# Performance work log

Hardware: AMD Instinct MI355X
Metric: run time of the kernel (lower is better)

## Reference

```python
import jax, jax.numpy as jnp
import numpy as np

NUM_CLASS = 4
K = 512
TEMP = 0.1
NEG_BIG = -1e9


def setup_inputs() -> dict:
    key = jax.random.key(0)
    ks = jax.random.split(key, 7)
    B, D, H, W = 8, 128, 128, 128
    return {
        "feat_x": jax.random.normal(ks[0], (B, D, H, W), jnp.float32),
        "pred_gt": jax.random.randint(ks[1], (B, H, W), 0, NUM_CLASS),
        "gt": jax.random.randint(ks[2], (B, H, W), 0, NUM_CLASS),
        "feat_u_s": jax.random.normal(ks[3], (B, D, H, W), jnp.float32),
        "feat_u_fp": jax.random.normal(ks[4], (B, D, H, W), jnp.float32),
        "logits_u": jax.random.uniform(ks[5], (B, H, W), jnp.float32),
        "label_u": jax.random.randint(ks[6], (B, H, W), 0, NUM_CLASS),
    }


def _rank_of_valid(mask, key):
    # Per-position rank under a random permutation; valid pixels get ranks [0, nv).
    r = jax.random.uniform(key, mask.shape)
    keys = jnp.where(mask, r, 2.0)  # invalid pixels sort last
    order = jnp.argsort(keys)
    return jnp.zeros_like(order).at[order].set(jnp.arange(order.shape[0]))


def _sample_feats(f_flat, mask, n, key):
    # f_flat: [N, D], mask: [N] bool -> feats [n+1, D] (n samples + class mean), valid [n+1]
    nv = mask.sum()
    order = jnp.argsort(jnp.where(mask, 0, 1))  # stable: valid pixel positions first
    u = jax.random.uniform(key, (n,))
    rand_idx = jnp.floor(u * nv).astype(jnp.int32)            # sample w/ replacement
    rep_idx = (jnp.arange(n) % jnp.maximum(nv, 1)).astype(jnp.int32)  # cyclic repeat
    idx = jnp.where(nv >= n, rand_idx, rep_idx)
    sampled = f_flat[order[idx]]                              # [n, D]
    mean = (f_flat * mask[:, None]).sum(0) / jnp.maximum(nv, 1)
    feats = jnp.concatenate([sampled, mean[None]], axis=0)
    valid = jnp.full((n + 1,), True) & (nv > 0)
    return feats, valid


def reference(feat_x, pred_gt, gt, feat_u_s, feat_u_fp, logits_u, label_u):
    # Label maps already at feature resolution -> nearest/bilinear resizes are identity.
    B, D, H, W = feat_x.shape
    N = B * H * W
    key = jax.random.key(42)
    base, rem = K // NUM_CLASS, K % NUM_CLASS

    f_l = feat_x.transpose(0, 2, 3, 1).reshape(N, D)
    f_s = feat_u_s.transpose(0, 2, 3, 1).reshape(N, D)
    f_fp = feat_u_fp.transpose(0, 2, 3, 1).reshape(N, D)
    pred_flat = pred_gt.reshape(N)
    lab_u_flat = label_u.reshape(N)
    log_u_flat = logits_u.reshape(N)
    thr = log_u_flat.mean()  # use_threshold=False -> dynamic mean threshold

    feats_l, valid_l, labels_l = [], [], []
    feats_u, valid_u, labels_u = [], [], []
    for cls in range(NUM_CLASS):
        n = base + (rem if cls == NUM_CLASS - 1 else 0)
        key, k1, k2, k3, k4 = jax.random.split(key, 5)
        # labeled: mask = pred == cls (use_TP=False)
        ml = pred_flat == cls
        fl, vl = _sample_feats(f_l, ml, n, k1)
        feats_l.append(fl); valid_l.append(vl)
        labels_l.append(jnp.full((n + 1,), cls, jnp.int32))
        # unlabeled: confident pixels of this class, randomly split into s / fp halves
        mu = (lab_u_flat == cls) & (log_u_flat >= thr)
        ranks = _rank_of_valid(mu, k2)
        half = mu.sum() // 2
        ms = mu & (ranks < half)
        mfp = mu & (ranks >= half)
        fs, vs = _sample_feats(f_s, ms, n, k3)
        ffp, vfp = _sample_feats(f_fp, mfp, n, k4)
        feats_u += [fs, ffp]; valid_u += [vs, vfp]
        labels_u.append(jnp.full((2 * (n + 1),), cls, jnp.int32))

    feat_l = jnp.concatenate(feats_l); val_l = jnp.concatenate(valid_l)
    lab_l = jnp.concatenate(labels_l)
    feat_u = jnp.concatenate(feats_u); val_u = jnp.concatenate(valid_u)
    labs_u = jnp.concatenate(labels_u)

    # InfoNCE over valid anchors/contrasts (validity mask replaces torch's NaN-row filtering)
    logits = feat_l @ feat_u.T / TEMP                      # [Kl, Ku]
    logits = jnp.where(val_u[None, :], logits, NEG_BIG)
    logits = logits - jax.lax.stop_gradient(logits.max(axis=1, keepdims=True))
    log_denom = jnp.log(jnp.exp(logits).sum(axis=1, keepdims=True))
    log_prob = jnp.where(val_u[None, :], logits - log_denom, 0.0)
    pos = ((lab_l[:, None] == labs_u[None, :]) & val_u[None, :]).astype(feat_l.dtype)
    mean_lpp = (pos * log_prob).sum(axis=1) / (pos.sum(axis=1) + 1e-12)
    loss = -(mean_lpp * val_l).sum() / jnp.maximum(val_l.sum(), 1)
    return jnp.where(val_l.any() & val_u.any(), loss, 0.0)
```

## Files before the change

### kernel.cpp

```cpp
#include <hip/hip_runtime.h>
#include <stdint.h>

#define N_PIX 131072
#define HW 16384
#define NSAMP 128
#define GSZ 129
#define ROWS_L 516
#define COLS_U 1032
#define INVALID_M 0xFFFFFFFFu

__host__ __device__ inline void tf2x32(uint32_t k0, uint32_t k1,
                                       uint32_t x0, uint32_t x1,
                                       uint32_t& o0, uint32_t& o1) {
  uint32_t ks2 = k0 ^ k1 ^ 0x1BD11BDAu;
  x0 += k0; x1 += k1;
#define TFR(r) { x0 += x1; x1 = (x1 << (r)) | (x1 >> (32 - (r))); x1 ^= x0; }
  TFR(13) TFR(15) TFR(26) TFR(6)   x0 += k1;  x1 += ks2 + 1u;
  TFR(17) TFR(29) TFR(16) TFR(24)  x0 += ks2; x1 += k0 + 2u;
  TFR(13) TFR(15) TFR(26) TFR(6)   x0 += k0;  x1 += k1 + 3u;
  TFR(17) TFR(29) TFR(16) TFR(24)  x0 += k1;  x1 += ks2 + 4u;
  TFR(13) TFR(15) TFR(26) TFR(6)   x0 += ks2; x1 += k0 + 5u;
#undef TFR
  o0 = x0; o1 = x1;
}

struct Keys4  { uint32_t a[4];  uint32_t b[4];  };
struct Keys12 { uint32_t a[12]; uint32_t b[12]; };

__global__ void k_sum(const float* __restrict__ x, double* out) {
  __shared__ double sm[256];
  int t = threadIdx.x;
  int base = blockIdx.x * 1024;
  double v = (double)x[base + t] + (double)x[base + 256 + t]
           + (double)x[base + 512 + t] + (double)x[base + 768 + t];
  sm[t] = v; __syncthreads();
  for (int o = 128; o > 0; o >>= 1) { if (t < o) sm[t] += sm[t + o]; __syncthreads(); }
  if (t == 0) atomicAdd(out, sm[0]);
}

__global__ void k_rankbits(const int* __restrict__ lab, const float* __restrict__ logu,
                           const double* __restrict__ sum, unsigned* __restrict__ m,
                           unsigned* __restrict__ cntu, Keys4 k2) {
  __shared__ unsigned cnt[4];
  int t = threadIdx.x;
  if (t < 4) cnt[t] = 0u;
  __syncthreads();
  int j = blockIdx.x * blockDim.x + t;
  double thr = (*sum) / 131072.0;
  int i0 = j, i1 = j + 65536;
  unsigned m0 = INVALID_M, m1 = INVALID_M;
  uint32_t o0, o1;
  if ((double)logu[i0] >= thr) {
    int c = lab[i0];
    tf2x32(k2.a[c], k2.b[c], (uint32_t)j, (uint32_t)(j + 65536), o0, o1);
    m0 = o0 >> 9; atomicAdd(&cnt[c], 1u);
  }
  if ((double)logu[i1] >= thr) {
    int c = lab[i1];
    tf2x32(k2.a[c], k2.b[c], (uint32_t)j, (uint32_t)(j + 65536), o0, o1);
    m1 = o1 >> 9; atomicAdd(&cnt[c], 1u);
  }
  m[i0] = m0; m[i1] = m1;
  __syncthreads();
  if (t < 4 && cnt[t] > 0u) atomicAdd(&cntu[t], cnt[t]);
}

__global__ void k_hist1(const int* __restrict__ lab, const unsigned* __restrict__ m,
                        unsigned* __restrict__ hist1) {
  int i = blockIdx.x * 256 + threadIdx.x;
  unsigned mi = m[i];
  if (mi != INVALID_M) atomicAdd(&hist1[lab[i] * 4096 + (mi >> 11)], 1u);
}

__global__ void k_scan1(const unsigned* __restrict__ hist1, const unsigned* __restrict__ cntu,
                        int* __restrict__ half_, int* __restrict__ bin_, int* __restrict__ base_) {
  int c = blockIdx.x, t = threadIdx.x;
  __shared__ unsigned part[256];
  const unsigned* h = hist1 + c * 4096;
  unsigned s = 0;
  for (int k = 0; k < 16; k++) s += h[t * 16 + k];
  part[t] = s; __syncthreads();
  if (t == 0) {
    int half = (int)(cntu[c] / 2u); half_[c] = half;
    if (half <= 0) { bin_[c] = -1; base_[c] = 0; }
    else {
      unsigned target = (unsigned)(half - 1), cum = 0; int pb = 0;
      for (; pb < 256; pb++) { if (cum + part[pb] > target) break; cum += part[pb]; }
      int b = pb * 16;
      for (;; b++) { unsigned hb = h[b]; if (cum + hb > target) break; cum += hb; }
      bin_[c] = b; base_[c] = (int)cum;
    }
  }
}

__global__ void k_hist2(const int* __restrict__ lab, const unsigned* __restrict__ m,
                        const int* __restrict__ bin_, unsigned* __restrict__ hist2) {
  int i = blockIdx.x * 256 + threadIdx.x;
  unsigned mi = m[i];
  if (mi == INVALID_M) return;
  int c = lab[i];
  if ((int)(mi >> 11) == bin_[c]) atomicAdd(&hist2[c * 2048 + (mi & 0x7FFu)], 1u);
}

__global__ void k_scan2(const unsigned* __restrict__ hist2, const int* __restrict__ half_,
                        const int* __restrict__ base_, const int* __restrict__ bin_,
                        unsigned* __restrict__ mstar_, int* __restrict__ t_) {
  int c = blockIdx.x, t = threadIdx.x;
  __shared__ unsigned part[256];
  const unsigned* h = hist2 + c * 2048;
  unsigned s = 0;
  for (int k = 0; k < 8; k++) s += h[t * 8 + k];
  part[t] = s; __syncthreads();
  if (t == 0) {
    int half = half_[c];
    if (half <= 0) { mstar_[c] = 0u; t_[c] = 0; }
    else {
      unsigned target = (unsigned)(half - 1), cum = (unsigned)base_[c]; int pb = 0;
      for (; pb < 256; pb++) { if (cum + part[pb] > target) break; cum += part[pb]; }
      int v = pb * 8;
      for (;; v++) { unsigned hb = h[v]; if (cum + hb > target) break; cum += hb; }
      mstar_[c] = ((unsigned)bin_[c] << 11) | (unsigned)v;
      t_[c] = half - (int)cum;
    }
  }
}

__global__ void k_ties(const int* __restrict__ lab, const unsigned* __restrict__ m,
                       const unsigned* __restrict__ mstar_, int* __restrict__ tiecnt,
                       int* __restrict__ tielist) {
  int i = blockIdx.x * 256 + threadIdx.x;
  unsigned mi = m[i];
  if (mi == INVALID_M) return;
  int c = lab[i];
  if (mi == mstar_[c]) {
    int p = atomicAdd(&tiecnt[c], 1);
    if (p < 128) tielist[c * 128 + p] = i;
  }
}

__global__ void k_tiesort(int* __restrict__ tielist, const int* __restrict__ tiecnt) {
  int c = threadIdx.x; if (c >= 4) return;
  int n = tiecnt[c]; if (n > 128) n = 128;
  int* L = tielist + c * 128;
  for (int a = 1; a < n; a++) {
    int x = L[a]; int b = a - 1;
    while (b >= 0 && L[b] > x) { L[b + 1] = L[b]; b--; }
    L[b + 1] = x;
  }
}

__global__ void k_split(const int* __restrict__ pred, const int* __restrict__ lab,
                        const unsigned* __restrict__ m, const unsigned* __restrict__ mstar_,
                        const int* __restrict__ t_, const int* __restrict__ tielist,
                        const int* __restrict__ tiecnt,
                        uint8_t* __restrict__ lgid, uint8_t* __restrict__ ugid,
                        unsigned* __restrict__ bc) {
  __shared__ unsigned cnt[12];
  int t = threadIdx.x;
  int i = blockIdx.x * 128 + t;
  if (t < 12) cnt[t] = 0u;
  __syncthreads();
  int pc = pred[i];
  lgid[i] = (uint8_t)pc;
  atomicAdd(&cnt[pc], 1u);
  unsigned mi = m[i];
  uint8_t ug = 255;
  if (mi != INVALID_M) {
    int c = lab[i];
    unsigned ms = mstar_[c];
    bool in_s;
    if (mi < ms) in_s = true;
    else if (mi > ms) in_s = false;
    else {
      int tc = tiecnt[c]; if (tc > 128) tc = 128;
      const int* L = tielist + c * 128;
      int rk = 0;
      for (int a = 0; a < tc; a++) if (L[a] < i) rk++;
      in_s = (rk < t_[c]);
    }
    ug = (uint8_t)((c << 1) + (in_s ? 0 : 1));
    atomicAdd(&cnt[4 + ug], 1u);
  }
  ugid[i] = ug;
  __syncthreads();
  if (t < 12) bc[t * 1024 + blockIdx.x] = cnt[t];
}

__global__ void k_scanblocks(const unsigned* __restrict__ bc, unsigned* __restrict__ offs,
                             unsigned* __restrict__ tot) {
  __shared__ unsigned wsum[16];
  int t = threadIdx.x;
  int lane = t & 63, w = t >> 6;
  for (int g = 0; g < 12; g++) {
    unsigned v = bc[g * 1024 + t];
    unsigned x = v;
    for (int o = 1; o < 64; o <<= 1) {
      unsigned y = __shfl_up(x, o, 64);
      if (lane >= o) x += y;
    }
    if (lane == 63) wsum[w] = x;
    __syncthreads();
    if (w == 0 && lane < 16) {
      unsigned s = wsum[lane];
      for (int o = 1; o < 16; o <<= 1) {
        unsigned y = __shfl_up(s, o, 64);
        if (lane >= o) s += y;
      }
      wsum[lane] = s;
    }
    __syncthreads();
    unsigned base = (w > 0) ? wsum[w - 1] : 0u;
    offs[g * 1024 + t] = base + x - v;
    if (t == 1023) tot[g] = base + x;
    __syncthreads();
  }
}

__global__ void k_sample(Keys12 gk, const unsigned* __restrict__ offs,
                         const unsigned* __restrict__ tot,
                         const uint8_t* __restrict__ lgid, const uint8_t* __restrict__ ugid,
                         int* __restrict__ sel) {
  int g = blockIdx.x, s = threadIdx.x;
  int nv = (int)tot[g];
  if (nv <= 0) { sel[g * 128 + s] = 0; return; }
  uint32_t o0, o1; int jj = s & 63;
  tf2x32(gk.a[g], gk.b[g], (uint32_t)jj, (uint32_t)(jj + 64), o0, o1);
  uint32_t bits = (s < 64) ? o0 : o1;
  float u = __uint_as_float((bits >> 9) | 0x3f800000u) - 1.0f;
  int q = (nv >= NSAMP) ? (int)floorf(u * (float)nv) : (s % nv);
  if (q > nv - 1) q = nv - 1;
  const unsigned* of = offs + g * 1024;
  int lo = 0, hi = 1023;
  while (lo < hi) { int mid = (lo + hi + 1) >> 1; if (of[mid] <= (unsigned)q) lo = mid; else hi = mid - 1; }
  int rem = q - (int)of[lo];
  const uint8_t* arr = (g < 4) ? lgid : ugid;
  uint8_t want = (g < 4) ? (uint8_t)g : (uint8_t)(g - 4);
  const unsigned* w32 = (const unsigned*)(arr + lo * 128);
  unsigned buf[32];
#pragma unroll
  for (int k = 0; k < 32; k++) buf[k] = w32[k];
  int found = 0;
  for (int k = 0; k < 128; k++) {
    uint8_t bb = (uint8_t)(buf[k >> 2] >> ((k & 3) * 8));
    if (bb == want) { if (rem == 0) { found = lo * 128 + k; break; } rem--; }
  }
  sel[g * 128 + s] = found;
}

__global__ void k_means(const float* __restrict__ fx, const float* __restrict__ fs,
                        const float* __restrict__ ffp,
                        const uint8_t* __restrict__ lgid, const uint8_t* __restrict__ ugid,
                        float* __restrict__ gsum) {
  int tensor = blockIdx.y;
  const float* f = (tensor == 0) ? fx : ((tensor == 1) ? fs : ffp);
  int b = blockIdx.x >> 7, d = blockIdx.x & 127;
  int t = threadIdx.x;
  int lane = t & 63, w = t >> 6;
  const float4* row4 = (const float4*)(f + ((size_t)(b * 128 + d)) * HW);
  const uchar4* gid4 = (const uchar4*)((tensor == 0 ? lgid : ugid) + (size_t)b * HW);
  int par = tensor - 1;
  float a0 = 0.f, a1 = 0.f, a2 = 0.f, a3 = 0.f;
#pragma unroll
  for (int i = 0; i < 16; i++) {
    int idx = i * 256 + t;
    float4 v = row4[idx];
    uchar4 gg = gid4[idx];
    int s0, s1, s2, s3;
    if (tensor == 0) { s0 = gg.x; s1 = gg.y; s2 = gg.z; s3 = gg.w; }
    else {
      s0 = (gg.x != 255 && (gg.x & 1) == par) ? (gg.x >> 1) : -1;
      s1 = (gg.y != 255 && (gg.y & 1) == par) ? (gg.y >> 1) : -1;
      s2 = (gg.z != 255 && (gg.z & 1) == par) ? (gg.z >> 1) : -1;
      s3 = (gg.w != 255 && (gg.w & 1) == par) ? (gg.w >> 1) : -1;
    }
    a0 += ((s0 == 0) ? v.x : 0.f) + ((s1 == 0) ? v.y : 0.f) + ((s2 == 0) ? v.z : 0.f) + ((s3 == 0) ? v.w : 0.f);
    a1 += ((s0 == 1) ? v.x : 0.f) + ((s1 == 1) ? v.y : 0.f) + ((s2 == 1) ? v.z : 0.f) + ((s3 == 1) ? v.w : 0.f);
    a2 += ((s0 == 2) ? v.x : 0.f) + ((s1 == 2) ? v.y : 0.f) + ((s2 == 2) ? v.z : 0.f) + ((s3 == 2) ? v.w : 0.f);
    a3 += ((s0 == 3) ? v.x : 0.f) + ((s1 == 3) ? v.y : 0.f) + ((s2 == 3) ? v.z : 0.f) + ((s3 == 3) ? v.w : 0.f);
  }
  for (int o = 32; o > 0; o >>= 1) {
    a0 += __shfl_xor(a0, o, 64);
    a1 += __shfl_xor(a1, o, 64);
    a2 += __shfl_xor(a2, o, 64);
    a3 += __shfl_xor(a3, o, 64);
  }
  __shared__ float swsum[4][4];
  if (lane == 0) { swsum[w][0] = a0; swsum[w][1] = a1; swsum[w][2] = a2; swsum[w][3] = a3; }
  __syncthreads();
  if (t < 4) {
    float v = swsum[0][t] + swsum[1][t] + swsum[2][t] + swsum[3][t];
    int g = (tensor == 0) ? t : (4 + (t << 1) + par);
    atomicAdd(&gsum[g * 128 + d], v);
  }
}

__global__ void k_gather(const float* __restrict__ fx, const float* __restrict__ fs,
                         const float* __restrict__ ffp, const int* __restrict__ sel,
                         const float* __restrict__ gsum, const unsigned* __restrict__ tot,
                         float* __restrict__ featl, float* __restrict__ featuT) {
  int r = blockIdx.x, d = threadIdx.x;
  const float* src; int g, s;
  if (r < ROWS_L) { g = r / GSZ; s = r - g * GSZ; src = fx; }
  else {
    int col = r - ROWS_L; int gu = col / GSZ; s = col - gu * GSZ;
    g = 4 + gu; src = (gu & 1) ? ffp : fs;
  }
  float val;
  if (s == NSAMP) {
    int nv = (int)tot[g]; if (nv < 1) nv = 1;
    val = gsum[g * 128 + d] / (float)nv;
  } else {
    int p = sel[g * 128 + s];
    int b = p >> 14, hw = p & 16383;
    val = src[((size_t)(b * 128 + d)) * HW + hw];
  }
  if (r < ROWS_L) featl[r * 128 + d] = val;
  else featuT[d * COLS_U + (r - ROWS_L)] = val;
}

__global__ void k_loss(const float* __restrict__ featl, const float* __restrict__ featuT,
                       const unsigned* __restrict__ tot, float* __restrict__ rowv) {
  int r = blockIdx.x, t = threadIdx.x;
  __shared__ float srow[128];
  __shared__ float slog[COLS_U];
  __shared__ float red[256];
  __shared__ float sbc[2];
  if (t < 128) srow[t] = featl[r * 128 + t];
  __syncthreads();
  for (int j = t; j < COLS_U; j += 256) {
    int gu = j / GSZ;
    float v;
    if (tot[4 + gu] > 0u) {
      float acc = 0.f;
      for (int d = 0; d < 128; d++) acc += srow[d] * featuT[d * COLS_U + j];
      v = acc / 0.1f;
    } else v = -1e9f;
    slog[j] = v;
  }
  __syncthreads();
  float mx = -3.4e38f;
  for (int j = t; j < COLS_U; j += 256) mx = fmaxf(mx, slog[j]);
  red[t] = mx; __syncthreads();
  for (int o = 128; o > 0; o >>= 1) { if (t < o) red[t] = fmaxf(red[t], red[t + o]); __syncthreads(); }
  if (t == 0) sbc[0] = red[0];
  __syncthreads();
  mx = sbc[0];
  float se = 0.f;
  for (int j = t; j < COLS_U; j += 256) se += expf(slog[j] - mx);
  red[t] = se; __syncthreads();
  for (int o = 128; o > 0; o >>= 1) { if (t < o) red[t] += red[t + o]; __syncthreads(); }
  if (t == 0) sbc[1] = logf(red[0]);
  __syncthreads();
  float logden = sbc[1];
  int myc = r / GSZ;
  float ps = 0.f, pl = 0.f;
  for (int j = t; j < COLS_U; j += 256) {
    int gu = j / GSZ;
    if (tot[4 + gu] > 0u && (gu >> 1) == myc) { ps += 1.f; pl += slog[j] - mx - logden; }
  }
  red[t] = ps; __syncthreads();
  for (int o = 128; o > 0; o >>= 1) { if (t < o) red[t] += red[t + o]; __syncthreads(); }
  float pst = red[0]; __syncthreads();
  red[t] = pl; __syncthreads();
  for (int o = 128; o > 0; o >>= 1) { if (t < o) red[t] += red[t + o]; __syncthreads(); }
  if (t == 0) rowv[r] = red[0] / (pst + 1e-12f);
}

__global__ void k_final(const float* __restrict__ rowv, const unsigned* __restrict__ tot,
                        float* __restrict__ out) {
  __shared__ float red[256];
  __shared__ float redc[256];
  int t = threadIdx.x;
  float s = 0.f, cn = 0.f;
  for (int r = t; r < ROWS_L; r += 256) {
    if (tot[r / GSZ] > 0u) { s += rowv[r]; cn += 1.f; }
  }
  red[t] = s; redc[t] = cn; __syncthreads();
  for (int o = 128; o > 0; o >>= 1) {
    if (t < o) { red[t] += red[t + o]; redc[t] += redc[t + o]; }
    __syncthreads();
  }
  if (t == 0) {
    bool anyL = (tot[0] | tot[1] | tot[2] | tot[3]) > 0u;
    bool anyU = false;
    for (int g = 4; g < 12; g++) anyU = anyU || (tot[g] > 0u);
    float loss = -red[0] / fmaxf(redc[0], 1.f);
    out[0] = (anyL && anyU) ? loss : 0.f;
  }
}

extern "C" void kernel_launch(void* const* d_in, const int* in_sizes, int n_in,
                              void* d_out, int out_size, void* d_ws, size_t ws_size,
                              hipStream_t stream) {
  const float* fx   = (const float*)d_in[0];
  const int*   pred = (const int*)d_in[1];
  const float* fs   = (const float*)d_in[3];
  const float* ffp  = (const float*)d_in[4];
  const float* logu = (const float*)d_in[5];
  const int*   lab  = (const int*)d_in[6];
  float* out = (float*)d_out;
  char* w = (char*)d_ws;

  uint32_t ka = 0u, kb = 42u;
  Keys4 K2; Keys12 GK;
  for (int c = 0; c < 4; c++) {
    uint32_t X0[5], X1[5];
    for (int j = 0; j < 5; j++) tf2x32(ka, kb, (uint32_t)j, (uint32_t)(j + 5), X0[j], X1[j]);
    uint32_t fl[10] = {X0[0],X0[1],X0[2],X0[3],X0[4],X1[0],X1[1],X1[2],X1[3],X1[4]};
    ka = fl[0]; kb = fl[1];
    GK.a[c] = fl[2];        GK.b[c] = fl[3];
    K2.a[c] = fl[4];        K2.b[c] = fl[5];
    GK.a[4 + 2*c] = fl[6];  GK.b[4 + 2*c] = fl[7];
    GK.a[5 + 2*c] = fl[8];  GK.b[5 + 2*c] = fl[9];
  }

  double*   d_sum    = (double*)(w + 0);
  unsigned* d_cntu   = (unsigned*)(w + 64);
  int*      d_half   = (int*)(w + 128);
  int*      d_bin    = (int*)(w + 192);
  int*      d_base   = (int*)(w + 256);
  unsigned* d_mstar  = (unsigned*)(w + 320);
  int*      d_tt     = (int*)(w + 384);
  int*      d_tiecnt = (int*)(w + 448);
  int*      d_tielist= (int*)(w + 512);
  unsigned* d_hist1  = (unsigned*)(w + 4096);
  unsigned* d_hist2  = (unsigned*)(w + 69632);
  unsigned* d_tot    = (unsigned*)(w + 102400);
  unsigned* d_bc     = (unsigned*)(w + 102656);
  unsigned* d_offs   = (unsigned*)(w + 151808);
  int*      d_sel    = (int*)(w + 200960);
  float*    d_gsum   = (float*)(w + 207104);
  unsigned* d_m      = (unsigned*)(w + 213248);
  uint8_t*  d_lgid   = (uint8_t*)(w + 737536);
  uint8_t*  d_ugid   = (uint8_t*)(w + 868608);
  float*    d_featl  = (float*)(w + 999680);
  float*    d_featuT = (float*)(w + 1263872);
  float*    d_rowv   = (float*)(w + 1792256);

  hipMemsetAsync(w, 0, 102400, stream);
  hipMemsetAsync(d_gsum, 0, 6144, stream);

  k_sum<<<128, 256, 0, stream>>>(logu, d_sum);
  k_rankbits<<<256, 256, 0, stream>>>(lab, logu, d_sum, d_m, d_cntu, K2);
  k_hist1<<<512, 256, 0, stream>>>(lab, d_m, d_hist1);
  k_scan1<<<4, 256, 0, stream>>>(d_hist1, d_cntu, d_half, d_bin, d_base);
  k_hist2<<<512, 256, 0, stream>>>(lab, d_m, d_bin, d_hist2);
  k_scan2<<<4, 256, 0, stream>>>(d_hist2, d_half, d_base, d_bin, d_mstar, d_tt);
  k_ties<<<512, 256, 0, stream>>>(lab, d_m, d_mstar, d_tiecnt, d_tielist);
  k_tiesort<<<1, 64, 0, stream>>>(d_tielist, d_tiecnt);
  k_split<<<1024, 128, 0, stream>>>(pred, lab, d_m, d_mstar, d_tt, d_tielist, d_tiecnt,
                                    d_lgid, d_ugid, d_bc);
  k_scanblocks<<<1, 1024, 0, stream>>>(d_bc, d_offs, d_tot);
  k_sample<<<12, 128, 0, stream>>>(GK, d_offs, d_tot, d_lgid, d_ugid, d_sel);
  k_means<<<dim3(1024, 3), 256, 0, stream>>>(fx, fs, ffp, d_lgid, d_ugid, d_gsum);
  k_gather<<<ROWS_L + COLS_U, 128, 0, stream>>>(fx, fs, ffp, d_sel, d_gsum, d_tot,
                                                d_featl, d_featuT);
  k_loss<<<ROWS_L, 256, 0, stream>>>(d_featl, d_featuT, d_tot, d_rowv);
  k_final<<<1, 256, 0, stream>>>(d_rowv, d_tot, out);
  (void)in_sizes; (void)n_in; (void)out_size; (void)ws_size;
}
```

Measured before the change: 340.7 us.

## Fuse pipeline stages with last-block-done reductions to cut kernel launches

Merges the histogram, scan, tie handling, block scan and sampling kernels into three kernels, each finishing with a last-block epilogue chosen by an atomic counter. The final loss reduction moves into the loss kernel the same way. The means kernel is split across twice as many blocks for more parallelism. The goal is to remove many small serial kernel launches and dependent round trips. In exchange, the tail work now runs serially in a single block, and the loss reductions switch to double precision.

```diff
diff --git a/kernel.cpp b/kernel.cpp
--- a/kernel.cpp
+++ b/kernel.cpp
@@ -27,6 +27,18 @@
 struct Keys4  { uint32_t a[4];  uint32_t b[4];  };
 struct Keys12 { uint32_t a[12]; uint32_t b[12]; };
 
+__device__ __forceinline__ bool last_block(unsigned* ctr, unsigned nblocks) {
+  __shared__ unsigned rk_;
+  __threadfence();
+  __syncthreads();
+  if (threadIdx.x == 0)
+    rk_ = __hip_atomic_fetch_add(ctr, 1u, __ATOMIC_ACQ_REL, __HIP_MEMORY_SCOPE_AGENT);
+  __syncthreads();
+  if (rk_ != nblocks - 1u) return false;
+  __threadfence();
+  return true;
+}
+
 __global__ void k_sum(const float* __restrict__ x, double* out) {
   __shared__ double sm[256];
   int t = threadIdx.x;
@@ -38,14 +50,16 @@
   if (t == 0) atomicAdd(out, sm[0]);
 }
 
-__global__ void k_rankbits(const int* __restrict__ lab, const float* __restrict__ logu,
-                           const double* __restrict__ sum, unsigned* __restrict__ m,
-                           unsigned* __restrict__ cntu, Keys4 k2) {
+__global__ void k_rank(const int* __restrict__ lab, const float* __restrict__ logu,
+                       const double* __restrict__ sum, unsigned* __restrict__ m,
+                       unsigned* __restrict__ cntu, unsigned* __restrict__ hist1,
+                       int* __restrict__ half_, int* __restrict__ bin_,
+                       int* __restrict__ base_, unsigned* __restrict__ ctr, Keys4 k2) {
   __shared__ unsigned cnt[4];
   int t = threadIdx.x;
   if (t < 4) cnt[t] = 0u;
   __syncthreads();
-  int j = blockIdx.x * blockDim.x + t;
+  int j = blockIdx.x * 256 + t;
   double thr = (*sum) / 131072.0;
   int i0 = j, i1 = j + 65536;
   unsigned m0 = INVALID_M, m1 = INVALID_M;
@@ -54,197 +68,195 @@
     int c = lab[i0];
     tf2x32(k2.a[c], k2.b[c], (uint32_t)j, (uint32_t)(j + 65536), o0, o1);
     m0 = o0 >> 9; atomicAdd(&cnt[c], 1u);
+    atomicAdd(&hist1[c * 4096 + (m0 >> 11)], 1u);
   }
   if ((double)logu[i1] >= thr) {
     int c = lab[i1];
     tf2x32(k2.a[c], k2.b[c], (uint32_t)j, (uint32_t)(j + 65536), o0, o1);
     m1 = o1 >> 9; atomicAdd(&cnt[c], 1u);
+    atomicAdd(&hist1[c * 4096 + (m1 >> 11)], 1u);
   }
   m[i0] = m0; m[i1] = m1;
   __syncthreads();
   if (t < 4 && cnt[t] > 0u) atomicAdd(&cntu[t], cnt[t]);
-}
-
-__global__ void k_hist1(const int* __restrict__ lab, const unsigned* __restrict__ m,
-                        unsigned* __restrict__ hist1) {
-  int i = blockIdx.x * 256 + threadIdx.x;
+
+  if (!last_block(ctr, gridDim.x)) return;
+  __shared__ unsigned part[256];
+  for (int c = 0; c < 4; c++) {
+    const unsigned* h = hist1 + c * 4096;
+    unsigned s = 0;
+    for (int k = 0; k < 16; k++) s += h[t * 16 + k];
+    part[t] = s; __syncthreads();
+    if (t == 0) {
+      int half = (int)(cntu[c] / 2u); half_[c] = half;
+      if (half <= 0) { bin_[c] = -1; base_[c] = 0; }
+      else {
+        unsigned target = (unsigned)(half - 1), cum = 0; int pb = 0;
+        for (; pb < 256; pb++) { if (cum + part[pb] > target) break; cum += part[pb]; }
+        int b = pb * 16;
+        for (;; b++) { unsigned hb = h[b]; if (cum + hb > target) break; cum += hb; }
+        bin_[c] = b; base_[c] = (int)cum;
+      }
+    }
+    __syncthreads();
+  }
+}
+
+__global__ void k_h2s2(const int* __restrict__ lab, const unsigned* __restrict__ m,
+                       const int* __restrict__ bin_, unsigned* __restrict__ hist2,
+                       const int* __restrict__ half_, const int* __restrict__ base_,
+                       unsigned* __restrict__ mstar_, int* __restrict__ t_,
+                       unsigned* __restrict__ ctr) {
+  int t = threadIdx.x;
+  int i = blockIdx.x * 256 + t;
   unsigned mi = m[i];
-  if (mi != INVALID_M) atomicAdd(&hist1[lab[i] * 4096 + (mi >> 11)], 1u);
-}
-
-__global__ void k_scan1(const unsigned* __restrict__ hist1, const unsigned* __restrict__ cntu,
-                        int* __restrict__ half_, int* __restrict__ bin_, int* __restrict__ base_) {
-  int c = blockIdx.x, t = threadIdx.x;
+  if (mi != INVALID_M) {
+    int c = lab[i];
+    if ((int)(mi >> 11) == bin_[c]) atomicAdd(&hist2[c * 2048 + (mi & 0x7FFu)], 1u);
+  }
+  if (!last_block(ctr, gridDim.x)) return;
   __shared__ unsigned part[256];
-  const unsigned* h = hist1 + c * 4096;
-  unsigned s = 0;
-  for (int k = 0; k < 16; k++) s += h[t * 16 + k];
-  part[t] = s; __syncthreads();
-  if (t == 0) {
-    int half = (int)(cntu[c] / 2u); half_[c] = half;
-    if (half <= 0) { bin_[c] = -1; base_[c] = 0; }
-    else {
-      unsigned target = (unsigned)(half - 1), cum = 0; int pb = 0;
-      for (; pb < 256; pb++) { if (cum + part[pb] > target) break; cum += part[pb]; }
-      int b = pb * 16;
-      for (;; b++) { unsigned hb = h[b]; if (cum + hb > target) break; cum += hb; }
-      bin_[c] = b; base_[c] = (int)cum;
-    }
-  }
-}
-
-__global__ void k_hist2(const int* __restrict__ lab, const unsigned* __restrict__ m,
-                        const int* __restrict__ bin_, unsigned* __restrict__ hist2) {
-  int i = blockIdx.x * 256 + threadIdx.x;
-  unsigned mi = m[i];
-  if (mi == INVALID_M) return;
-  int c = lab[i];
-  if ((int)(mi >> 11) == bin_[c]) atomicAdd(&hist2[c * 2048 + (mi & 0x7FFu)], 1u);
-}
-
-__global__ void k_scan2(const unsigned* __restrict__ hist2, const int* __restrict__ half_,
-                        const int* __restrict__ base_, const int* __restrict__ bin_,
-                        unsigned* __restrict__ mstar_, int* __restrict__ t_) {
-  int c = blockIdx.x, t = threadIdx.x;
-  __shared__ unsigned part[256];
-  const unsigned* h = hist2 + c * 2048;
-  unsigned s = 0;
-  for (int k = 0; k < 8; k++) s += h[t * 8 + k];
-  part[t] = s; __syncthreads();
-  if (t == 0) {
-    int half = half_[c];
-    if (half <= 0) { mstar_[c] = 0u; t_[c] = 0; }
-    else {
-      unsigned target = (unsigned)(half - 1), cum = (unsigned)base_[c]; int pb = 0;
-      for (; pb < 256; pb++) { if (cum + part[pb] > target) break; cum += part[pb]; }
-      int v = pb * 8;
-      for (;; v++) { unsigned hb = h[v]; if (cum + hb > target) break; cum += hb; }
-      mstar_[c] = ((unsigned)bin_[c] << 11) | (unsigned)v;
-      t_[c] = half - (int)cum;
-    }
-  }
-}
-
-__global__ void k_ties(const int* __restrict__ lab, const unsigned* __restrict__ m,
-                       const unsigned* __restrict__ mstar_, int* __restrict__ tiecnt,
-                       int* __restrict__ tielist) {
-  int i = blockIdx.x * 256 + threadIdx.x;
-  unsigned mi = m[i];
-  if (mi == INVALID_M) return;
-  int c = lab[i];
-  if (mi == mstar_[c]) {
-    int p = atomicAdd(&tiecnt[c], 1);
-    if (p < 128) tielist[c * 128 + p] = i;
-  }
-}
-
-__global__ void k_tiesort(int* __restrict__ tielist, const int* __restrict__ tiecnt) {
-  int c = threadIdx.x; if (c >= 4) return;
-  int n = tiecnt[c]; if (n > 128) n = 128;
-  int* L = tielist + c * 128;
-  for (int a = 1; a < n; a++) {
-    int x = L[a]; int b = a - 1;
-    while (b >= 0 && L[b] > x) { L[b + 1] = L[b]; b--; }
-    L[b + 1] = x;
-  }
-}
-
-__global__ void k_split(const int* __restrict__ pred, const int* __restrict__ lab,
-                        const unsigned* __restrict__ m, const unsigned* __restrict__ mstar_,
-                        const int* __restrict__ t_, const int* __restrict__ tielist,
-                        const int* __restrict__ tiecnt,
-                        uint8_t* __restrict__ lgid, uint8_t* __restrict__ ugid,
-                        unsigned* __restrict__ bc) {
+  for (int c = 0; c < 4; c++) {
+    const unsigned* h = hist2 + c * 2048;
+    unsigned s = 0;
+    for (int k = 0; k < 8; k++) s += h[t * 8 + k];
+    part[t] = s; __syncthreads();
+    if (t == 0) {
+      int half = half_[c];
+      if (half <= 0) { mstar_[c] = 0u; t_[c] = 0; }
+      else {
+        unsigned target = (unsigned)(half - 1), cum = (unsigned)base_[c]; int pb = 0;
+        for (; pb < 256; pb++) { if (cum + part[pb] > target) break; cum += part[pb]; }
+        int v = pb * 8;
+        for (;; v++) { unsigned hb = h[v]; if (cum + hb > target) break; cum += hb; }
+        mstar_[c] = ((unsigned)bin_[c] << 11) | (unsigned)v;
+        t_[c] = half - (int)cum;
+      }
+    }
+    __syncthreads();
+  }
+}
+
+__global__ void k_part(const int* __restrict__ pred, const int* __restrict__ lab,
+                       const unsigned* __restrict__ m, const unsigned* __restrict__ mstar_,
+                       const int* __restrict__ t_, int* __restrict__ tiecnt,
+                       int* __restrict__ tielist,
+                       uint8_t* __restrict__ lgid, uint8_t* __restrict__ ugid,
+                       unsigned* __restrict__ bc, unsigned* __restrict__ totg,
+                       int* __restrict__ sel, unsigned* __restrict__ ctr, Keys12 gk) {
   __shared__ unsigned cnt[12];
   int t = threadIdx.x;
-  int i = blockIdx.x * 128 + t;
+  int lane = t & 63, w = t >> 6;
+  int i = blockIdx.x * 256 + t;
   if (t < 12) cnt[t] = 0u;
   __syncthreads();
   int pc = pred[i];
   lgid[i] = (uint8_t)pc;
   atomicAdd(&cnt[pc], 1u);
   unsigned mi = m[i];
-  uint8_t ug = 255;
+  int ug = 255;
   if (mi != INVALID_M) {
     int c = lab[i];
     unsigned ms = mstar_[c];
-    bool in_s;
-    if (mi < ms) in_s = true;
-    else if (mi > ms) in_s = false;
+    if (mi < ms) ug = (c << 1);
+    else if (mi > ms) ug = (c << 1) + 1;
     else {
-      int tc = tiecnt[c]; if (tc > 128) tc = 128;
-      const int* L = tielist + c * 128;
+      int p = atomicAdd(&tiecnt[c], 1);
+      if (p < 128) tielist[c * 128 + p] = i;
+      ug = 254;
+    }
+    if (ug < 8) atomicAdd(&cnt[4 + ug], 1u);
+  }
+  ugid[i] = (uint8_t)ug;
+  __syncthreads();
+  if (t < 12) bc[t * 512 + blockIdx.x] = cnt[t];
+
+  if (!last_block(ctr, gridDim.x)) return;
+
+  __shared__ unsigned sbc[12][512];
+  __shared__ unsigned stot[12];
+  __shared__ unsigned wtot[4];
+  for (int k = t; k < 12 * 512; k += 256) ((unsigned*)sbc)[k] = bc[k];
+  __syncthreads();
+  for (int c = 0; c < 4; c++) {
+    int tc = tiecnt[c]; if (tc > 128) tc = 128;
+    int tcv = t_[c];
+    for (int a = t; a < tc; a += 256) {
+      int i2 = tielist[c * 128 + a];
       int rk = 0;
-      for (int a = 0; a < tc; a++) if (L[a] < i) rk++;
-      in_s = (rk < t_[c]);
-    }
-    ug = (uint8_t)((c << 1) + (in_s ? 0 : 1));
-    atomicAdd(&cnt[4 + ug], 1u);
-  }
-  ugid[i] = ug;
-  __syncthreads();
-  if (t < 12) bc[t * 1024 + blockIdx.x] = cnt[t];
-}
-
-__global__ void k_scanblocks(const unsigned* __restrict__ bc, unsigned* __restrict__ offs,
-                             unsigned* __restrict__ tot) {
-  __shared__ unsigned wsum[16];
-  int t = threadIdx.x;
-  int lane = t & 63, w = t >> 6;
+      for (int b2 = 0; b2 < tc; b2++) rk += (tielist[c * 128 + b2] < i2);
+      int ug2 = (c << 1) + ((rk < tcv) ? 0 : 1);
+      ugid[i2] = (uint8_t)ug2;
+      atomicAdd(&sbc[4 + ug2][i2 >> 8], 1u);
+    }
+  }
+  __syncthreads();
   for (int g = 0; g < 12; g++) {
-    unsigned v = bc[g * 1024 + t];
-    unsigned x = v;
+    unsigned v0 = sbc[g][2 * t], v1 = sbc[g][2 * t + 1];
+    unsigned s2 = v0 + v1, x = s2;
     for (int o = 1; o < 64; o <<= 1) {
       unsigned y = __shfl_up(x, o, 64);
       if (lane >= o) x += y;
     }
-    if (lane == 63) wsum[w] = x;
+    if (lane == 63) wtot[w] = x;
     __syncthreads();
-    if (w == 0 && lane < 16) {
-      unsigned s = wsum[lane];
-      for (int o = 1; o < 16; o <<= 1) {
-        unsigned y = __shfl_up(s, o, 64);
-        if (lane >= o) s += y;
+    unsigned base = 0;
+    for (int ww = 0; ww < 4; ww++) if (ww < w) base += wtot[ww];
+    unsigned excl = base + x - s2;
+    sbc[g][2 * t] = excl; sbc[g][2 * t + 1] = excl + v0;
+    if (t == 255) stot[g] = excl + v0 + v1;
+    __syncthreads();
+  }
+  if (t < 12) totg[t] = stot[t];
+  __syncthreads();
+  for (int k = 0; k < 6; k++) {
+    int idx = k * 256 + t;
+    int g = idx >> 7, s = idx & 127;
+    int nv = (int)stot[g];
+    int res = 0;
+    if (nv > 0) {
+      uint32_t o0, o1; int jj = s & 63;
+      tf2x32(gk.a[g], gk.b[g], (uint32_t)jj, (uint32_t)(jj + 64), o0, o1);
+      uint32_t bits = (s < 64) ? o0 : o1;
+      float u = __uint_as_float((bits >> 9) | 0x3f800000u) - 1.0f;
+      int q = (nv >= NSAMP) ? (int)floorf(u * (float)nv) : (s % nv);
+      if (q > nv - 1) q = nv - 1;
+      int lo = 0, hi = 511;
+      while (lo < hi) { int mid = (lo + hi + 1) >> 1; if (sbc[g][mid] <= (unsigned)q) lo = mid; else hi = mid - 1; }
+      int rem = q - (int)sbc[g][lo];
+      const uint8_t* arr = (g < 4) ? lgid : ugid;
+      unsigned want = (g < 4) ? (unsigned)g : (unsigned)(g - 4);
+      const unsigned* w32 = (const unsigned*)(arr + lo * 256);
+      int found = -1;
+      for (int ch = 0; ch < 4; ch++) {
+        if (found >= 0) break;
+        unsigned buf[16];
+#pragma unroll
+        for (int q2 = 0; q2 < 16; q2++) buf[q2] = w32[ch * 16 + q2];
+        int mcnt = 0;
+#pragma unroll
+        for (int q2 = 0; q2 < 16; q2++) {
+          unsigned bb = buf[q2];
+          mcnt += (int)((bb & 255u) == want) + (int)(((bb >> 8) & 255u) == want)
+                + (int)(((bb >> 16) & 255u) == want) + (int)(((bb >> 24) & 255u) == want);
+        }
+        if (rem >= mcnt) { rem -= mcnt; continue; }
+#pragma unroll
+        for (int q2 = 0; q2 < 16; q2++) {
+          unsigned bb = buf[q2];
+#pragma unroll
+          for (int b3 = 0; b3 < 4; b3++) {
+            if (found < 0 && ((bb >> (8 * b3)) & 255u) == want) {
+              if (rem == 0) found = lo * 256 + ch * 64 + q2 * 4 + b3;
+              else rem--;
+            }
+          }
+        }
       }
-      wsum[lane] = s;
-    }
-    __syncthreads();
-    unsigned base = (w > 0) ? wsum[w - 1] : 0u;
-    offs[g * 1024 + t] = base + x - v;
-    if (t == 1023) tot[g] = base + x;
-    __syncthreads();
-  }
-}
-
-__global__ void k_sample(Keys12 gk, const unsigned* __restrict__ offs,
-                         const unsigned* __restrict__ tot,
-                         const uint8_t* __restrict__ lgid, const uint8_t* __restrict__ ugid,
-                         int* __restrict__ sel) {
-  int g = blockIdx.x, s = threadIdx.x;
-  int nv = (int)tot[g];
-  if (nv <= 0) { sel[g * 128 + s] = 0; return; }
-  uint32_t o0, o1; int jj = s & 63;
-  tf2x32(gk.a[g], gk.b[g], (uint32_t)jj, (uint32_t)(jj + 64), o0, o1);
-  uint32_t bits = (s < 64) ? o0 : o1;
-  float u = __uint_as_float((bits >> 9) | 0x3f800000u) - 1.0f;
-  int q = (nv >= NSAMP) ? (int)floorf(u * (float)nv) : (s % nv);
-  if (q > nv - 1) q = nv - 1;
-  const unsigned* of = offs + g * 1024;
-  int lo = 0, hi = 1023;
-  while (lo < hi) { int mid = (lo + hi + 1) >> 1; if (of[mid] <= (unsigned)q) lo = mid; else hi = mid - 1; }
-  int rem = q - (int)of[lo];
-  const uint8_t* arr = (g < 4) ? lgid : ugid;
-  uint8_t want = (g < 4) ? (uint8_t)g : (uint8_t)(g - 4);
-  const unsigned* w32 = (const unsigned*)(arr + lo * 128);
-  unsigned buf[32];
-#pragma unroll
-  for (int k = 0; k < 32; k++) buf[k] = w32[k];
-  int found = 0;
-  for (int k = 0; k < 128; k++) {
-    uint8_t bb = (uint8_t)(buf[k >> 2] >> ((k & 3) * 8));
-    if (bb == want) { if (rem == 0) { found = lo * 128 + k; break; } rem--; }
-  }
-  sel[g * 128 + s] = found;
+      res = (found >= 0) ? found : 0;
+    }
+    sel[g * 128 + s] = res;
+  }
 }
 
 __global__ void k_means(const float* __restrict__ fx, const float* __restrict__ fs,
@@ -253,25 +265,27 @@
                         float* __restrict__ gsum) {
   int tensor = blockIdx.y;
   const float* f = (tensor == 0) ? fx : ((tensor == 1) ? fs : ffp);
-  int b = blockIdx.x >> 7, d = blockIdx.x & 127;
+  int rb = blockIdx.x >> 1;
+  int half = blockIdx.x & 1;
+  int b = rb >> 7, d = rb & 127;
   int t = threadIdx.x;
   int lane = t & 63, w = t >> 6;
-  const float4* row4 = (const float4*)(f + ((size_t)(b * 128 + d)) * HW);
-  const uchar4* gid4 = (const uchar4*)((tensor == 0 ? lgid : ugid) + (size_t)b * HW);
+  const float4* row4 = (const float4*)(f + ((size_t)(b * 128 + d)) * HW) + half * 2048;
+  const uchar4* gid4 = (const uchar4*)((tensor == 0 ? lgid : ugid) + (size_t)b * HW) + half * 2048;
   int par = tensor - 1;
   float a0 = 0.f, a1 = 0.f, a2 = 0.f, a3 = 0.f;
 #pragma unroll
-  for (int i = 0; i < 16; i++) {
+  for (int i = 0; i < 8; i++) {
     int idx = i * 256 + t;
     float4 v = row4[idx];
     uchar4 gg = gid4[idx];
     int s0, s1, s2, s3;
     if (tensor == 0) { s0 = gg.x; s1 = gg.y; s2 = gg.z; s3 = gg.w; }
     else {
-      s0 = (gg.x != 255 && (gg.x & 1) == par) ? (gg.x >> 1) : -1;
-      s1 = (gg.y != 255 && (gg.y & 1) == par) ? (gg.y >> 1) : -1;
-      s2 = (gg.z != 255 && (gg.z & 1) == par) ? (gg.z >> 1) : -1;
-      s3 = (gg.w != 255 && (gg.w & 1) == par) ? (gg.w >> 1) : -1;
+      s0 = (gg.x < 8 && (gg.x & 1) == par) ? (gg.x >> 1) : -1;
+      s1 = (gg.y < 8 && (gg.y & 1) == par) ? (gg.y >> 1) : -1;
+      s2 = (gg.z < 8 && (gg.z & 1) == par) ? (gg.z >> 1) : -1;
+      s3 = (gg.w < 8 && (gg.w & 1) == par) ? (gg.w >> 1) : -1;
     }
     a0 += ((s0 == 0) ? v.x : 0.f) + ((s1 == 0) ? v.y : 0.f) + ((s2 == 0) ? v.z : 0.f) + ((s3 == 0) ? v.w : 0.f);
     a1 += ((s0 == 1) ? v.x : 0.f) + ((s1 == 1) ? v.y : 0.f) + ((s2 == 1) ? v.z : 0.f) + ((s3 == 1) ? v.w : 0.f);
@@ -319,12 +333,15 @@
 }
 
 __global__ void k_loss(const float* __restrict__ featl, const float* __restrict__ featuT,
-                       const unsigned* __restrict__ tot, float* __restrict__ rowv) {
+                       const unsigned* __restrict__ tot, float* __restrict__ rowv,
+                       unsigned* __restrict__ ctr, float* __restrict__ out) {
   int r = blockIdx.x, t = threadIdx.x;
   __shared__ float srow[128];
   __shared__ float slog[COLS_U];
   __shared__ float red[256];
-  __shared__ float sbc[2];
+  __shared__ double dred[256];
+  __shared__ float sm_;
+  __shared__ double sld;
   if (t < 128) srow[t] = featl[r * 128 + t];
   __syncthreads();
   for (int j = t; j < COLS_U; j += 256) {
@@ -342,50 +359,47 @@
   for (int j = t; j < COLS_U; j += 256) mx = fmaxf(mx, slog[j]);
   red[t] = mx; __syncthreads();
   for (int o = 128; o > 0; o >>= 1) { if (t < o) red[t] = fmaxf(red[t], red[t + o]); __syncthreads(); }
-  if (t == 0) sbc[0] = red[0];
-  __syncthreads();
-  mx = sbc[0];
-  float se = 0.f;
-  for (int j = t; j < COLS_U; j += 256) se += expf(slog[j] - mx);
-  red[t] = se; __syncthreads();
-  for (int o = 128; o > 0; o >>= 1) { if (t < o) red[t] += red[t + o]; __syncthreads(); }
-  if (t == 0) sbc[1] = logf(red[0]);
-  __syncthreads();
-  float logden = sbc[1];
+  if (t == 0) sm_ = red[0];
+  __syncthreads();
+  mx = sm_;
+  double se = 0.0;
+  for (int j = t; j < COLS_U; j += 256) se += (double)expf(slog[j] - mx);
+  dred[t] = se; __syncthreads();
+  for (int o = 128; o > 0; o >>= 1) { if (t < o) dred[t] += dred[t + o]; __syncthreads(); }
+  if (t == 0) sld = log(dred[0]);
+  __syncthreads();
+  double logden = sld;
   int myc = r / GSZ;
-  float ps = 0.f, pl = 0.f;
+  double ps = 0.0, pl = 0.0;
   for (int j = t; j < COLS_U; j += 256) {
     int gu = j / GSZ;
-    if (tot[4 + gu] > 0u && (gu >> 1) == myc) { ps += 1.f; pl += slog[j] - mx - logden; }
-  }
-  red[t] = ps; __syncthreads();
-  for (int o = 128; o > 0; o >>= 1) { if (t < o) red[t] += red[t + o]; __syncthreads(); }
-  float pst = red[0]; __syncthreads();
-  red[t] = pl; __syncthreads();
-  for (int o = 128; o > 0; o >>= 1) { if (t < o) red[t] += red[t + o]; __syncthreads(); }
-  if (t == 0) rowv[r] = red[0] / (pst + 1e-12f);
-}
-
-__global__ void k_final(const float* __restrict__ rowv, const unsigned* __restrict__ tot,
-                        float* __restrict__ out) {
-  __shared__ float red[256];
-  __shared__ float redc[256];
-  int t = threadIdx.x;
-  float s = 0.f, cn = 0.f;
-  for (int r = t; r < ROWS_L; r += 256) {
-    if (tot[r / GSZ] > 0u) { s += rowv[r]; cn += 1.f; }
-  }
-  red[t] = s; redc[t] = cn; __syncthreads();
+    if (tot[4 + gu] > 0u && (gu >> 1) == myc) {
+      ps += 1.0; pl += (double)slog[j] - (double)mx - logden;
+    }
+  }
+  dred[t] = ps; __syncthreads();
+  for (int o = 128; o > 0; o >>= 1) { if (t < o) dred[t] += dred[t + o]; __syncthreads(); }
+  double pst = dred[0]; __syncthreads();
+  dred[t] = pl; __syncthreads();
+  for (int o = 128; o > 0; o >>= 1) { if (t < o) dred[t] += dred[t + o]; __syncthreads(); }
+  if (t == 0) rowv[r] = (float)(dred[0] / (pst + 1e-12));
+
+  if (!last_block(ctr, gridDim.x)) return;
+  double s = 0.0, cn = 0.0;
+  for (int r2 = t; r2 < ROWS_L; r2 += 256) {
+    if (tot[r2 / GSZ] > 0u) { s += (double)rowv[r2]; cn += 1.0; }
+  }
+  dred[t] = s; red[t] = (float)cn; __syncthreads();
   for (int o = 128; o > 0; o >>= 1) {
-    if (t < o) { red[t] += red[t + o]; redc[t] += redc[t + o]; }
+    if (t < o) { dred[t] += dred[t + o]; red[t] += red[t + o]; }
     __syncthreads();
   }
   if (t == 0) {
     bool anyL = (tot[0] | tot[1] | tot[2] | tot[3]) > 0u;
     bool anyU = false;
     for (int g = 4; g < 12; g++) anyU = anyU || (tot[g] > 0u);
-    float loss = -red[0] / fmaxf(redc[0], 1.f);
-    out[0] = (anyL && anyU) ? loss : 0.f;
+    double loss = -dred[0] / ((red[0] > 1.f) ? (double)red[0] : 1.0);
+    out[0] = (anyL && anyU) ? (float)loss : 0.f;
   }
 }
 
@@ -422,40 +436,33 @@
   unsigned* d_mstar  = (unsigned*)(w + 320);
   int*      d_tt     = (int*)(w + 384);
   int*      d_tiecnt = (int*)(w + 448);
-  int*      d_tielist= (int*)(w + 512);
+  unsigned* d_ctr    = (unsigned*)(w + 512);
+  int*      d_tielist= (int*)(w + 1024);
   unsigned* d_hist1  = (unsigned*)(w + 4096);
   unsigned* d_hist2  = (unsigned*)(w + 69632);
-  unsigned* d_tot    = (unsigned*)(w + 102400);
-  unsigned* d_bc     = (unsigned*)(w + 102656);
-  unsigned* d_offs   = (unsigned*)(w + 151808);
-  int*      d_sel    = (int*)(w + 200960);
-  float*    d_gsum   = (float*)(w + 207104);
-  unsigned* d_m      = (unsigned*)(w + 213248);
-  uint8_t*  d_lgid   = (uint8_t*)(w + 737536);
-  uint8_t*  d_ugid   = (uint8_t*)(w + 868608);
-  float*    d_featl  = (float*)(w + 999680);
-  float*    d_featuT = (float*)(w + 1263872);
-  float*    d_rowv   = (float*)(w + 1792256);
-
-  hipMemsetAsync(w, 0, 102400, stream);
-  hipMemsetAsync(d_gsum, 0, 6144, stream);
+  float*    d_gsum   = (float*)(w + 102400);
+  unsigned* d_tot    = (unsigned*)(w + 108544);
+  unsigned* d_bc     = (unsigned*)(w + 108608);
+  int*      d_sel    = (int*)(w + 133184);
+  unsigned* d_m      = (unsigned*)(w + 139328);
+  uint8_t*  d_lgid   = (uint8_t*)(w + 663616);
+  uint8_t*  d_ugid   = (uint8_t*)(w + 794688);
+  float*    d_featl  = (float*)(w + 925760);
+  float*    d_featuT = (float*)(w + 1189952);
+  float*    d_rowv   = (float*)(w + 1718336);
+
+  hipMemsetAsync(w, 0, 108544, stream);
 
   k_sum<<<128, 256, 0, stream>>>(logu, d_sum);
-  k_rankbits<<<256, 256, 0, stream>>>(lab, logu, d_sum, d_m, d_cntu, K2);
-  k_hist1<<<512, 256, 0, stream>>>(lab, d_m, d_hist1);
-  k_scan1<<<4, 256, 0, stream>>>(d_hist1, d_cntu, d_half, d_bin, d_base);
-  k_hist2<<<512, 256, 0, stream>>>(lab, d_m, d_bin, d_hist2);
-  k_scan2<<<4, 256, 0, stream>>>(d_hist2, d_half, d_base, d_bin, d_mstar, d_tt);
-  k_ties<<<512, 256, 0, stream>>>(lab, d_m, d_mstar, d_tiecnt, d_tielist);
-  k_tiesort<<<1, 64, 0, stream>>>(d_tielist, d_tiecnt);
-  k_split<<<1024, 128, 0, stream>>>(pred, lab, d_m, d_mstar, d_tt, d_tielist, d_tiecnt,
-                                    d_lgid, d_ugid, d_bc);
-  k_scanblocks<<<1, 1024, 0, stream>>>(d_bc, d_offs, d_tot);
-  k_sample<<<12, 128, 0, stream>>>(GK, d_offs, d_tot, d_lgid, d_ugid, d_sel);
-  k_means<<<dim3(1024, 3), 256, 0, stream>>>(fx, fs, ffp, d_lgid, d_ugid, d_gsum);
+  k_rank<<<256, 256, 0, stream>>>(lab, logu, d_sum, d_m, d_cntu, d_hist1,
+                                  d_half, d_bin, d_base, &d_ctr[0], K2);
+  k_h2s2<<<512, 256, 0, stream>>>(lab, d_m, d_bin, d_hist2, d_half, d_base,
+                                  d_mstar, d_tt, &d_ctr[1]);
+  k_part<<<512, 256, 0, stream>>>(pred, lab, d_m, d_mstar, d_tt, d_tiecnt, d_tielist,
+                                  d_lgid, d_ugid, d_bc, d_tot, d_sel, &d_ctr[2], GK);
+  k_means<<<dim3(2048, 3), 256, 0, stream>>>(fx, fs, ffp, d_lgid, d_ugid, d_gsum);
   k_gather<<<ROWS_L + COLS_U, 128, 0, stream>>>(fx, fs, ffp, d_sel, d_gsum, d_tot,
                                                 d_featl, d_featuT);
-  k_loss<<<ROWS_L, 256, 0, stream>>>(d_featl, d_featuT, d_tot, d_rowv);
-  k_final<<<1, 256, 0, stream>>>(d_rowv, d_tot, out);
+  k_loss<<<ROWS_L, 256, 0, stream>>>(d_featl, d_featuT, d_tot, d_rowv, &d_ctr[3], out);
   (void)in_sizes; (void)n_in; (void)out_size; (void)ws_size;
 }
```

New measurement: 560.7 us. +64.6%, slower.
